# Kernel optimization log

Hardware: AMD Instinct MI355X
Metric: run time of the kernel (lower is better)

## Reference

```python
import jax, jax.numpy as jnp
import numpy as np

N, E, D, H = 50000, 800000, 64, 64  # nodes, edges, in_dim, hid_dim


def setup_inputs() -> dict:
    key = jax.random.key(0)
    ks = jax.random.split(key, 16)
    s = lambda fan_in: 1.0 / np.sqrt(fan_in)
    inp = {
        "node_feat": jax.random.normal(ks[0], (N, D), jnp.float32),
        "coord": jax.random.normal(ks[1], (N, 3), jnp.float32),
        "edge_list": jax.random.randint(ks[2], (E, 2), 0, N, jnp.int32),
        # edge_mlp: Linear(2D+1 -> H), Linear(H -> H)
        "We1": jax.random.normal(ks[3], (2 * D + 1, H), jnp.float32) * s(2 * D + 1),
        "be1": jnp.zeros((H,), jnp.float32),
        "We2": jax.random.normal(ks[4], (H, H), jnp.float32) * s(H),
        "be2": jnp.zeros((H,), jnp.float32),
        # node_mlp: Linear(H+D -> H), Linear(H -> H)
        "Wn1": jax.random.normal(ks[5], (H + D, H), jnp.float32) * s(H + D),
        "bn1": jnp.zeros((H,), jnp.float32),
        "Wn2": jax.random.normal(ks[6], (H, H), jnp.float32) * s(H),
        "bn2": jnp.zeros((H,), jnp.float32),
        # coord_mlp: Linear(H -> H), Linear(H -> 1, bias=False, xavier gain 1e-3)
        "Wc1": jax.random.normal(ks[7], (H, H), jnp.float32) * s(H),
        "bc1": jnp.zeros((H,), jnp.float32),
        "wc": jax.random.normal(ks[8], (H, 1), jnp.float32) * 0.001,
    }
    return inp


def reference(node_feat, coord, edge_list, We1, be1, We2, be2,
              Wn1, bn1, Wn2, bn2, Wc1, bc1, wc):
    n = node_feat.shape[0]
    node_in = edge_list[:, 0]
    node_out = edge_list[:, 1]

    # coord2radial (normalize=False)
    coord_diff = coord[node_out] - coord[node_in]            # [E,3]
    radial = jnp.sum(coord_diff * coord_diff, axis=1, keepdims=True)  # [E,1]

    # edge_function (no edge_attr, no attention)
    edge_in = jnp.concatenate(
        [node_feat[node_in], node_feat[node_out], radial], axis=1)    # [E,2D+1]
    h = jax.nn.relu(edge_in @ We1 + be1)
    edge_feat = jax.nn.relu(h @ We2 + be2)                   # [E,H]

    # coord_function, coords_agg='mean'
    trans_w = jax.nn.relu(edge_feat @ Wc1 + bc1) @ wc        # [E,1]
    weighted_trans = coord_diff * trans_w                    # [E,3]
    agg = jax.ops.segment_sum(weighted_trans, node_out, num_segments=n)
    cnt = jax.ops.segment_sum(jnp.ones((node_out.shape[0],), coord.dtype),
                              node_out, num_segments=n)
    coord_out = coord + agg / jnp.maximum(cnt, 1.0)[:, None]

    # node_function (residual, dims match)
    agg_edge = jax.ops.segment_sum(edge_feat, node_out, num_segments=n)  # [N,H]
    node_in_feat = jnp.concatenate([node_feat, agg_edge], axis=1)
    nf = jax.nn.relu(node_in_feat @ Wn1 + bn1) @ Wn2 + bn2
    node_feat_out = node_feat + nf

    return node_feat_out, coord_out
```

## Files before the change

kernel.cpp:

```cpp
#include <hip/hip_runtime.h>
#include <hip/hip_fp8.h>

#define NN 50000
#define NE 800000
#define PREP_BLOCKS 784
#define PREP_THREADS (PREP_BLOCKS * 256)

typedef __bf16 bf16x8 __attribute__((ext_vector_type(8)));
typedef float  f32x4  __attribute__((ext_vector_type(4)));

__device__ __forceinline__ float frelu(float x) { return fmaxf(x, 0.f); }

__device__ __forceinline__ float fp8_to_f32(unsigned char b) {
    __hip_fp8_e4m3 t; t.__x = (__hip_fp8_storage_t)b; return (float)t;
}
__device__ __forceinline__ unsigned char f32_to_fp8(float f) {
    return (unsigned char)__hip_fp8_e4m3(f).__x;
}

__global__ __launch_bounds__(256) void prep_kernel(
    const float* __restrict__ nf, const int* __restrict__ el,
    const float* __restrict__ We1, const float* __restrict__ We2,
    const float* __restrict__ Wc1, const float* __restrict__ Wn1,
    const float* __restrict__ Wn2, const float* __restrict__ be1,
    __bf16* __restrict__ W2T,  __bf16* __restrict__ Wc1T,
    __bf16* __restrict__ Wn1T, __bf16* __restrict__ Wn2T,
    unsigned char* __restrict__ Pa, __bf16* __restrict__ Pb,
    int* __restrict__ deg, int* __restrict__ rank, float* __restrict__ agg_edge)
{
    __shared__ __align__(16) __bf16 w1lds[64 * 128];
    if (blockIdx.x < 196) {
        for (int idx = threadIdx.x; idx < 64 * 128; idx += 256) {
            const int k = idx >> 6;
            const int j = idx & 63;
            w1lds[j * 128 + (k ^ ((j & 7) << 3))] = (__bf16)We1[k * 64 + j];
        }
    }

    const int tid = blockIdx.x * 256 + threadIdx.x;

    if (tid < 4096) {
        const int j = tid & 63, k = tid >> 6;
        W2T [j * 64 + k] = (__bf16)We2[k * 64 + j];
        Wc1T[j * 64 + k] = (__bf16)Wc1[k * 64 + j];
        Wn2T[j * 64 + k] = (__bf16)Wn2[k * 64 + j];
        Wn1T[j * 128 + k]      = (__bf16)Wn1[k * 64 + j];
        Wn1T[j * 128 + 64 + k] = (__bf16)Wn1[(64 + k) * 64 + j];
    }

    {
        const f32x4 z = (f32x4){0.f, 0.f, 0.f, 0.f};
        for (int i = tid; i < NN * 16; i += PREP_THREADS)
            ((f32x4*)agg_edge)[i] = z;
    }

    for (int e = tid; e < NE; e += PREP_THREADS) {
        const int2 pr = ((const int2*)el)[e];
        rank[e] = atomicAdd(&deg[pr.y], 1);
    }

    if (blockIdx.x >= 196) return;
    __syncthreads();

    const int w = threadIdx.x >> 6, lane = threadIdx.x & 63;
    const int c = lane & 15, g = lane >> 4;
    const int mbase = blockIdx.x * 256 + w * 64;

    bf16x8 af[4][2];
#pragma unroll
    for (int m = 0; m < 4; ++m) {
        int node = mbase + m * 16 + c;
        node = (node < NN) ? node : (NN - 1);
#pragma unroll
        for (int s = 0; s < 2; ++s) {
            const int k0 = s * 32 + g * 8;
            const float4 v0 = *(const float4*)(nf + (size_t)node * 64 + k0);
            const float4 v1 = *(const float4*)(nf + (size_t)node * 64 + k0 + 4);
            bf16x8 a;
            a[0] = (__bf16)v0.x; a[1] = (__bf16)v0.y; a[2] = (__bf16)v0.z; a[3] = (__bf16)v0.w;
            a[4] = (__bf16)v1.x; a[5] = (__bf16)v1.y; a[6] = (__bf16)v1.z; a[7] = (__bf16)v1.w;
            af[m][s] = a;
        }
    }

    {
        f32x4 cc[4][4];
#pragma unroll
        for (int m = 0; m < 4; ++m)
#pragma unroll
            for (int n = 0; n < 4; ++n) cc[m][n] = (f32x4){0.f, 0.f, 0.f, 0.f};
#pragma unroll
        for (int n = 0; n < 4; ++n)
#pragma unroll
            for (int s = 0; s < 2; ++s) {
                const int j = n * 16 + c;
                const bf16x8 b = *(const bf16x8*)&w1lds[j * 128 + ((s * 32 + g * 8) ^ ((j & 7) << 3))];
#pragma unroll
                for (int m = 0; m < 4; ++m)
                    cc[m][n] = __builtin_amdgcn_mfma_f32_16x16x32_bf16(af[m][s], b, cc[m][n], 0, 0, 0);
            }
#pragma unroll
        for (int m = 0; m < 4; ++m)
#pragma unroll
            for (int n = 0; n < 4; ++n)
#pragma unroll
                for (int r = 0; r < 4; ++r) {
                    const int node = mbase + m * 16 + g * 4 + r;
                    if (node < NN) Pa[(size_t)node * 64 + n * 16 + c] = f32_to_fp8(cc[m][n][r]);
                }
    }
    {
        f32x4 cc[4][4];
#pragma unroll
        for (int m = 0; m < 4; ++m)
#pragma unroll
            for (int n = 0; n < 4; ++n) cc[m][n] = (f32x4){0.f, 0.f, 0.f, 0.f};
#pragma unroll
        for (int n = 0; n < 4; ++n)
#pragma unroll
            for (int s = 0; s < 2; ++s) {
                const int j = n * 16 + c;
                const bf16x8 b = *(const bf16x8*)&w1lds[j * 128 + 64 + ((s * 32 + g * 8) ^ ((j & 7) << 3))];
#pragma unroll
                for (int m = 0; m < 4; ++m)
                    cc[m][n] = __builtin_amdgcn_mfma_f32_16x16x32_bf16(af[m][s], b, cc[m][n], 0, 0, 0);
            }
#pragma unroll
        for (int n = 0; n < 4; ++n) {
            const float bb = be1[n * 16 + c];
#pragma unroll
            for (int m = 0; m < 4; ++m)
#pragma unroll
                for (int r = 0; r < 4; ++r) {
                    const int node = mbase + m * 16 + g * 4 + r;
                    if (node < NN) Pb[(size_t)node * 64 + n * 16 + c] = (__bf16)(cc[m][n][r] + bb);
                }
        }
    }
}

__global__ __launch_bounds__(256) void alloc1_kernel(
    const int* __restrict__ deg, int* __restrict__ base_rel,
    int* __restrict__ chunkSum)
{
    __shared__ int wsum[4];
    const int t = threadIdx.x;
    const int n = blockIdx.x * 256 + t;
    const int lid = t & 63, wid = t >> 6;
    const int d = (n < NN) ? deg[n] : 0;
    int pre = d;
#pragma unroll
    for (int off = 1; off < 64; off <<= 1) {
        const int v = __shfl_up(pre, off);
        if (lid >= off) pre += v;
    }
    if (lid == 63) wsum[wid] = pre;
    __syncthreads();
    int woff = 0;
#pragma unroll
    for (int i = 0; i < 4; ++i) if (i < wid) woff += wsum[i];
    if (n < NN) base_rel[n] = woff + pre - d;
    if (t == 255) chunkSum[blockIdx.x] = woff + pre;
}

__global__ __launch_bounds__(256) void alloc2_kernel(
    const int* __restrict__ chunkSum, int* __restrict__ chunkOff)
{
    __shared__ int s[256];
    const int t = threadIdx.x;
    const int v0 = (t < 196) ? chunkSum[t] : 0;
    s[t] = v0;
    __syncthreads();
    for (int d = 1; d < 256; d <<= 1) {
        const int v = (t >= d) ? s[t - d] : 0;
        __syncthreads();
        s[t] += v;
        __syncthreads();
    }
    if (t < 196) chunkOff[t] = s[t] - v0;
}

__global__ __launch_bounds__(256) void scatter_kernel(
    const int* __restrict__ el, const int* __restrict__ base_rel,
    const int* __restrict__ chunkOff, const int* __restrict__ rank,
    int2* __restrict__ sorted_el, float* __restrict__ agg3)
{
    const int e = blockIdx.x * 256 + threadIdx.x;
    if (e < NN * 3) agg3[e] = 0.f;
    const int2 pr = ((const int2*)el)[e];
    sorted_el[chunkOff[pr.y >> 8] + base_rel[pr.y] + rank[e]] = pr;
}

__global__ __launch_bounds__(128, 4) void edge_mfma(
    const unsigned char* __restrict__ Pa, const __bf16* __restrict__ Pb,
    const float* __restrict__ coord, const int2* __restrict__ sorted_el,
    const float* __restrict__ We1,
    const __bf16* __restrict__ W2T, const float* __restrict__ be2,
    const __bf16* __restrict__ Wc1T, const float* __restrict__ bc1,
    const float* __restrict__ wc,
    float* __restrict__ agg_edge, float* __restrict__ agg3)
{
    __shared__ __align__(16) __bf16 tile[2][64 * 32];
    __shared__ int   nout_s[2][64];
    __shared__ float tw_s[2][64];

    const int w    = threadIdx.x >> 6;
    const int lane = threadIdx.x & 63;
    const int c    = lane & 15;
    const int g    = lane >> 4;
    const int ebase = blockIdx.x * 128 + w * 64;

    const int2 pr = sorted_el[ebase + lane];
    const int nin = pr.x, nout = pr.y;
    nout_s[w][lane] = nout;
    const float cdx = coord[3 * nout + 0] - coord[3 * nin + 0];
    const float cdy = coord[3 * nout + 1] - coord[3 * nin + 1];
    const float cdz = coord[3 * nout + 2] - coord[3 * nin + 2];
    const float radial = cdx * cdx + cdy * cdy + cdz * cdz;

    float wv[2][8];
#pragma unroll
    for (int s = 0; s < 2; ++s) {
        const int k0 = s * 32 + g * 8;
        const float4 a = *(const float4*)(We1 + 128 * 64 + k0);
        const float4 b = *(const float4*)(We1 + 128 * 64 + k0 + 4);
        wv[s][0] = a.x; wv[s][1] = a.y; wv[s][2] = a.z; wv[s][3] = a.w;
        wv[s][4] = b.x; wv[s][5] = b.y; wv[s][6] = b.z; wv[s][7] = b.w;
    }

    bf16x8 af[4][2];
#pragma unroll
    for (int m = 0; m < 4; ++m) {
        const int e   = m * 16 + c;
        const int ni  = __shfl(nin, e);
        const int no  = __shfl(nout, e);
        const float rad = __shfl(radial, e);
        const unsigned char* paRow = Pa + (size_t)ni * 64;
        const __bf16* pbRow = Pb + (size_t)no * 64;
#pragma unroll
        for (int s = 0; s < 2; ++s) {
            const int k0 = s * 32 + g * 8;
            const uint2 pu = *(const uint2*)(paRow + k0);
            const bf16x8 pb = *(const bf16x8*)(pbRow + k0);
            bf16x8 a;
#pragma unroll
            for (int i = 0; i < 8; ++i) {
                const unsigned char pbyte =
                    (unsigned char)(((i < 4 ? pu.x : pu.y) >> (8 * (i & 3))) & 0xFF);
                a[i] = (__bf16)frelu(fp8_to_f32(pbyte) + (float)pb[i] + rad * wv[s][i]);
            }
            af[m][s] = a;
        }
    }

    bf16x8 a2[4][2];
#pragma unroll
    for (int p = 0; p < 2; ++p) {
        f32x4 c1h[4][2];
#pragma unroll
        for (int q = 0; q < 2; ++q) {
            const float b = be2[(2 * p + q) * 16 + c];
#pragma unroll
            for (int m = 0; m < 4; ++m) c1h[m][q] = (f32x4){b, b, b, b};
        }
#pragma unroll
        for (int q = 0; q < 2; ++q)
#pragma unroll
            for (int s = 0; s < 2; ++s) {
                const bf16x8 b = *(const bf16x8*)(W2T + ((2 * p + q) * 16 + c) * 64 + s * 32 + g * 8);
#pragma unroll
                for (int m = 0; m < 4; ++m)
                    c1h[m][q] = __builtin_amdgcn_mfma_f32_16x16x32_bf16(af[m][s], b, c1h[m][q], 0, 0, 0);
            }

#pragma unroll
        for (int m = 0; m < 4; ++m)
#pragma unroll
            for (int q = 0; q < 2; ++q)
#pragma unroll
                for (int r = 0; r < 4; ++r) {
                    const int e = m * 16 + g * 4 + r;
                    const int lc = q * 16 + c;
                    tile[w][e * 32 + (lc ^ (((e >> 1) & 3) << 3))] = (__bf16)frelu(c1h[m][q][r]);
                }

#pragma unroll
        for (int m = 0; m < 4; ++m) {
            const int e = m * 16 + c;
            a2[m][p] = *(const bf16x8*)&tile[w][e * 32 + ((g * 8) ^ (((e >> 1) & 3) << 3))];
        }

        {
            const int lc = lane & 31;
            const int rbase = (lane >> 5) * 32;
            int cur = nout_s[w][rbase];
            float acc = 0.f;
#pragma unroll 4
            for (int rr = 0; rr < 32; ++rr) {
                const int r = rbase + rr;
                acc += (float)tile[w][r * 32 + (lc ^ (((r >> 1) & 3) << 3))];
                const int nxt = (rr < 31) ? nout_s[w][r + 1] : -1;
                if (nxt != cur) {
                    atomicAdd(&agg_edge[(size_t)cur * 64 + p * 32 + lc], acc);
                    acc = 0.f;
                    cur = nxt;
                }
            }
        }
    }

    f32x4 twp[4];
#pragma unroll
    for (int m = 0; m < 4; ++m) twp[m] = (f32x4){0.f, 0.f, 0.f, 0.f};
#pragma unroll
    for (int n = 0; n < 4; ++n) {
        const float b = bc1[n * 16 + c];
        const float wn = wc[n * 16 + c];
        f32x4 c2[4];
#pragma unroll
        for (int m = 0; m < 4; ++m) c2[m] = (f32x4){b, b, b, b};
#pragma unroll
        for (int s = 0; s < 2; ++s) {
            const bf16x8 bb = *(const bf16x8*)(Wc1T + (n * 16 + c) * 64 + s * 32 + g * 8);
#pragma unroll
            for (int m = 0; m < 4; ++m)
                c2[m] = __builtin_amdgcn_mfma_f32_16x16x32_bf16(a2[m][s], bb, c2[m], 0, 0, 0);
        }
#pragma unroll
        for (int m = 0; m < 4; ++m)
#pragma unroll
            for (int r = 0; r < 4; ++r)
                twp[m][r] = fmaf(frelu(c2[m][r]), wn, twp[m][r]);
    }

#pragma unroll
    for (int m = 0; m < 4; ++m) {
#pragma unroll
        for (int r = 0; r < 4; ++r) {
            float p = twp[m][r];
            p += __shfl_xor(p, 1);
            p += __shfl_xor(p, 2);
            p += __shfl_xor(p, 4);
            p += __shfl_xor(p, 8);
            if (c == 0) tw_s[w][m * 16 + g * 4 + r] = p;
        }
    }

    {
        const bool act = (lane < 48);
        const int dim = lane % 3;
        const int chunk = act ? (lane / 3) : 0;
        const int r0 = chunk * 4;
        int cur = nout_s[w][r0];
        float acc = 0.f;
#pragma unroll
        for (int rr = 0; rr < 4; ++rr) {
            const int r = r0 + rr;
            const float sx = __shfl(cdx, r);
            const float sy = __shfl(cdy, r);
            const float sz = __shfl(cdz, r);
            const float cdv = (dim == 0) ? sx : (dim == 1) ? sy : sz;
            acc += cdv * tw_s[w][r];
            const int nxt = (rr < 3) ? nout_s[w][r + 1] : -1;
            if (nxt != cur) {
                if (act) atomicAdd(&agg3[3 * cur + dim], acc);
                acc = 0.f;
                cur = nxt;
            }
        }
    }
}

__global__ __launch_bounds__(128) void node_mfma(
    const float* __restrict__ nf, const float* __restrict__ coord,
    const float* __restrict__ agg_edge, const int* __restrict__ deg,
    float* agg3_coordout,
    const __bf16* __restrict__ Wn1T, const float* __restrict__ bn1,
    const __bf16* __restrict__ Wn2T, const float* __restrict__ bn2,
    float* __restrict__ out_feat)
{
    __shared__ __align__(16) __bf16 tile[2][64 * 64];
    const int t = threadIdx.x;
    const int w = t >> 6, lane = t & 63, c = lane & 15, g = lane >> 4;
    const int nblk = blockIdx.x * 128;

    const int nodeT = nblk + t;
    if (nodeT < NN) {
        const float invc = 1.f / fmaxf((float)deg[nodeT], 1.f);
#pragma unroll
        for (int d = 0; d < 3; ++d) {
            const float a = agg3_coordout[3 * nodeT + d];
            agg3_coordout[3 * nodeT + d] = coord[3 * nodeT + d] + a * invc;
        }
    }

    const int mbase = nblk + w * 64;

    bf16x8 a1[4][4];
#pragma unroll
    for (int m = 0; m < 4; ++m) {
        int node = mbase + m * 16 + c;
        node = (node < NN) ? node : (NN - 1);
#pragma unroll
        for (int s = 0; s < 4; ++s) {
            const int k0 = s * 32 + g * 8;
            const float* src = (k0 < 64) ? (nf + (size_t)node * 64 + k0)
                                         : (agg_edge + (size_t)node * 64 + (k0 - 64));
            const float4 v0 = *(const float4*)src;
            const float4 v1 = *(const float4*)(src + 4);
            bf16x8 a;
            a[0] = (__bf16)v0.x; a[1] = (__bf16)v0.y; a[2] = (__bf16)v0.z; a[3] = (__bf16)v0.w;
            a[4] = (__bf16)v1.x; a[5] = (__bf16)v1.y; a[6] = (__bf16)v1.z; a[7] = (__bf16)v1.w;
            a1[m][s] = a;
        }
    }

    f32x4 c1[4][4];
#pragma unroll
    for (int n = 0; n < 4; ++n) {
        const float b = bn1[n * 16 + c];
#pragma unroll
        for (int m = 0; m < 4; ++m) c1[m][n] = (f32x4){b, b, b, b};
    }
#pragma unroll
    for (int n = 0; n < 4; ++n)
#pragma unroll
        for (int s = 0; s < 4; ++s) {
            const bf16x8 b = *(const bf16x8*)(Wn1T + (n * 16 + c) * 128 + s * 32 + g * 8);
#pragma unroll
            for (int m = 0; m < 4; ++m)
                c1[m][n] = __builtin_amdgcn_mfma_f32_16x16x32_bf16(a1[m][s], b, c1[m][n], 0, 0, 0);
        }

#pragma unroll
    for (int m = 0; m < 4; ++m)
#pragma unroll
        for (int n = 0; n < 4; ++n)
#pragma unroll
            for (int r = 0; r < 4; ++r) {
                const int e = m * 16 + g * 4 + r;
                tile[w][e * 64 + ((n * 16 + c) ^ ((e & 7) << 3))] = (__bf16)frelu(c1[m][n][r]);
            }

    bf16x8 a2[4][2];
#pragma unroll
    for (int m = 0; m < 4; ++m) {
        const int e = m * 16 + c;
#pragma unroll
        for (int s = 0; s < 2; ++s) {
            const int k0 = s * 32 + g * 8;
            a2[m][s] = *(const bf16x8*)&tile[w][e * 64 + (k0 ^ ((e & 7) << 3))];
        }
    }
    f32x4 c2[4][4];
#pragma unroll
    for (int n = 0; n < 4; ++n) {
        const float b = bn2[n * 16 + c];
#pragma unroll
        for (int m = 0; m < 4; ++m) c2[m][n] = (f32x4){b, b, b, b};
    }
#pragma unroll
    for (int n = 0; n < 4; ++n)
#pragma unroll
        for (int s = 0; s < 2; ++s) {
            const bf16x8 b = *(const bf16x8*)(Wn2T + (n * 16 + c) * 64 + s * 32 + g * 8);
#pragma unroll
            for (int m = 0; m < 4; ++m)
                c2[m][n] = __builtin_amdgcn_mfma_f32_16x16x32_bf16(a2[m][s], b, c2[m][n], 0, 0, 0);
        }

#pragma unroll
    for (int m = 0; m < 4; ++m)
#pragma unroll
        for (int n = 0; n < 4; ++n)
#pragma unroll
            for (int r = 0; r < 4; ++r) {
                const int node = mbase + m * 16 + g * 4 + r;
                if (node < NN) {
                    const int col = n * 16 + c;
                    out_feat[(size_t)node * 64 + col] =
                        nf[(size_t)node * 64 + col] + c2[m][n][r];
                }
            }
}

extern "C" void kernel_launch(void* const* d_in, const int* in_sizes, int n_in,
                              void* d_out, int out_size, void* d_ws, size_t ws_size,
                              hipStream_t stream)
{
    const float* nf    = (const float*)d_in[0];
    const float* coord = (const float*)d_in[1];
    const int*   el    = (const int*)d_in[2];
    const float* We1   = (const float*)d_in[3];
    const float* be1   = (const float*)d_in[4];
    const float* We2   = (const float*)d_in[5];
    const float* be2   = (const float*)d_in[6];
    const float* Wn1   = (const float*)d_in[7];
    const float* bn1   = (const float*)d_in[8];
    const float* Wn2   = (const float*)d_in[9];
    const float* bn2   = (const float*)d_in[10];
    const float* Wc1   = (const float*)d_in[11];
    const float* bc1   = (const float*)d_in[12];
    const float* wc    = (const float*)d_in[13];

    float* out_feat  = (float*)d_out;
    float* out_coord = out_feat + (size_t)NN * 64;

    unsigned char* Pa = (unsigned char*)d_out;
    int*    rank = (int*)((char*)d_out + 3200000);
    float*  agg3 = out_coord;

    char* ws = (char*)d_ws;
    __bf16* Pb       = (__bf16*)ws;
    float* agg_edge  = (float*)(ws + 6400000);
    int*   deg       = (int*)(ws + 19200000);
    int*   base_rel  = (int*)(ws + 19400000);
    int2*  sorted_el = (int2*)(ws + 19600000);
    __bf16* W2T  = (__bf16*)(ws + 26000000);
    __bf16* Wc1T = W2T + 4096;
    __bf16* Wn2T = Wc1T + 4096;
    __bf16* Wn1T = Wn2T + 4096;
    int*   chunkSum = (int*)(ws + 26041088);
    int*   chunkOff = (int*)(ws + 26042112);

    hipMemsetAsync(deg, 0, (size_t)NN * sizeof(int), stream);

    prep_kernel<<<dim3(PREP_BLOCKS), dim3(256), 0, stream>>>(
        nf, el, We1, We2, Wc1, Wn1, Wn2, be1,
        W2T, Wc1T, Wn1T, Wn2T,
        Pa, Pb, deg, rank, agg_edge);

    alloc1_kernel<<<dim3(196), dim3(256), 0, stream>>>(deg, base_rel, chunkSum);
    alloc2_kernel<<<dim3(1), dim3(256), 0, stream>>>(chunkSum, chunkOff);

    scatter_kernel<<<dim3(NE / 256), dim3(256), 0, stream>>>(
        el, base_rel, chunkOff, rank, sorted_el, agg3);

    edge_mfma<<<dim3(NE / 128), dim3(128), 0, stream>>>(
        Pa, Pb, coord, sorted_el, We1, W2T, be2, Wc1T, bc1, wc,
        agg_edge, agg3);

    node_mfma<<<dim3((NN + 127) / 128), dim3(128), 0, stream>>>(
        nf, coord, agg_edge, deg, agg3, Wn1T, bn1, Wn2T, bn2, out_feat);
}
```

Before: 167.3 us.

## Permute edge-to-row mapping so segmented reduction runs from MFMA registers

Reorders which edge each MFMA row handles so each lane's accumulator fragment holds 16 consecutive sorted edges. The agg_edge segmented sum can then read directly from the c1h registers, using destination ids preloaded by shuffles, instead of reading back the LDS tile and an LDS array of destination ids. The coordinate reduction is remapped to the permuted tw_s layout and takes its ids from shuffles. This removes LDS traffic and the 32-step serial loop, but adds 16 registers per lane and two atomics per fragment column. Segments now break at 16-edge groups instead of 32, which may mean more atomics.

```diff
diff --git a/kernel.cpp b/kernel.cpp
--- a/kernel.cpp
+++ b/kernel.cpp
@@ -201,7 +201,6 @@
     float* __restrict__ agg_edge, float* __restrict__ agg3)
 {
     __shared__ __align__(16) __bf16 tile[2][64 * 32];
-    __shared__ int   nout_s[2][64];
     __shared__ float tw_s[2][64];
 
     const int w    = threadIdx.x >> 6;
@@ -212,11 +211,14 @@
 
     const int2 pr = sorted_el[ebase + lane];
     const int nin = pr.x, nout = pr.y;
-    nout_s[w][lane] = nout;
     const float cdx = coord[3 * nout + 0] - coord[3 * nin + 0];
     const float cdy = coord[3 * nout + 1] - coord[3 * nin + 1];
     const float cdz = coord[3 * nout + 2] - coord[3 * nin + 2];
     const float radial = cdx * cdx + cdy * cdy + cdz * cdz;
+
+    int nw[16];
+#pragma unroll
+    for (int o = 0; o < 16; ++o) nw[o] = __shfl(nout, g * 16 + o);
 
     float wv[2][8];
 #pragma unroll
@@ -231,7 +233,7 @@
     bf16x8 af[4][2];
 #pragma unroll
     for (int m = 0; m < 4; ++m) {
-        const int e   = m * 16 + c;
+        const int e   = ((c >> 2) << 4) + (m << 2) + (c & 3);
         const int ni  = __shfl(nin, e);
         const int no  = __shfl(nout, e);
         const float rad = __shfl(radial, e);
@@ -290,18 +292,17 @@
             a2[m][p] = *(const bf16x8*)&tile[w][e * 32 + ((g * 8) ^ (((e >> 1) & 3) << 3))];
         }
 
-        {
-            const int lc = lane & 31;
-            const int rbase = (lane >> 5) * 32;
-            int cur = nout_s[w][rbase];
+#pragma unroll
+        for (int q = 0; q < 2; ++q) {
+            const int colIdx = (2 * p + q) * 16 + c;
+            int cur = nw[0];
             float acc = 0.f;
-#pragma unroll 4
-            for (int rr = 0; rr < 32; ++rr) {
-                const int r = rbase + rr;
-                acc += (float)tile[w][r * 32 + (lc ^ (((r >> 1) & 3) << 3))];
-                const int nxt = (rr < 31) ? nout_s[w][r + 1] : -1;
+#pragma unroll
+            for (int o = 0; o < 16; ++o) {
+                acc += frelu(c1h[o >> 2][q][o & 3]);
+                const int nxt = (o < 15) ? nw[o + 1] : -1;
                 if (nxt != cur) {
-                    atomicAdd(&agg_edge[(size_t)cur * 64 + p * 32 + lc], acc);
+                    atomicAdd(&agg_edge[(size_t)cur * 64 + colIdx], acc);
                     acc = 0.f;
                     cur = nxt;
                 }
@@ -351,7 +352,7 @@
         const int dim = lane % 3;
         const int chunk = act ? (lane / 3) : 0;
         const int r0 = chunk * 4;
-        int cur = nout_s[w][r0];
+        int cur = __shfl(nout, r0);
         float acc = 0.f;
 #pragma unroll
         for (int rr = 0; rr < 4; ++rr) {
@@ -360,8 +361,10 @@
             const float sy = __shfl(cdy, r);
             const float sz = __shfl(cdz, r);
             const float cdv = (dim == 0) ? sx : (dim == 1) ? sy : sz;
-            acc += cdv * tw_s[w][r];
-            const int nxt = (rr < 3) ? nout_s[w][r + 1] : -1;
+            const int rho = 16 * ((r >> 2) & 3) + 4 * (r >> 4) + (r & 3);
+            acc += cdv * tw_s[w][rho];
+            int nxt = -1;
+            if (rr < 3) nxt = __shfl(nout, r + 1);
             if (nxt != cur) {
                 if (act) atomicAdd(&agg3[3 * cur + dim], acc);
                 acc = 0.f;
```

Result: slower. 177.2 us (+5.9%).
